# Optimization experiments

Measured on AMD Instinct MI355X. Metric: run time of the kernel, lower is better.

Reference implementation:

```python
import jax, jax.numpy as jnp
import numpy as np

B, N, C, H = 2, 8192, 256, 8  # Dh == C (attention_head_size = embedding_channels)
EPS = 1e-5  # InstanceNorm2d default eps


def setup_inputs() -> dict:
    key = jax.random.key(0)
    k1, k2, k3, k4, k5 = jax.random.split(key, 5)
    s = 1.0 / np.sqrt(C)
    return {
        "emb": jax.random.normal(k1, (B, N, C), dtype=jnp.float32),
        "Wq": jax.random.normal(k2, (C, C * H), dtype=jnp.float32) * s,
        "Wk": jax.random.normal(k3, (C, C * H), dtype=jnp.float32) * s,
        "Wv": jax.random.normal(k4, (C, C * H), dtype=jnp.float32) * s,
        "Wo": jax.random.normal(k5, (C * H, C), dtype=jnp.float32) * s,
    }


def reference(emb, Wq, Wk, Wv, Wo):
    b, n, c = emb.shape
    h = Wq.shape[1] // c  # num_heads; head_dim Dh == c

    def heads(x):  # [B,N,H*Dh] -> [B,H,N,Dh]
        return x.reshape(b, n, h, c).transpose(0, 2, 1, 3)

    qh = heads(emb @ Wq)  # [B,H,N,Dh]
    kh = heads(emb @ Wk)
    vh = heads(emb @ Wv)

    # channel attention: contract over sequence dim N -> [B,H,Dh,Dh]
    attn = jnp.einsum("bhnd,bhne->bhde", qh, kh)

    # InstanceNorm2d over the Dh x Dh map per (b,h), affine=False, biased var
    mu = attn.mean(axis=(2, 3), keepdims=True)
    var = attn.var(axis=(2, 3), keepdims=True)
    attn = (attn - mu) * jax.lax.rsqrt(var + EPS)

    attn = jax.nn.softmax(attn, axis=3)

    # attn @ v^T -> [B,H,Dh,N]
    ctx = jnp.einsum("bhde,bhne->bhdn", attn, vh)

    # permute(0,3,2,1) -> [B,N,Dh,H], flatten (Dh,H) -> KV_size
    ctx = ctx.transpose(0, 3, 2, 1).reshape(b, n, c * h)
    return ctx @ Wo  # [B,N,C]
```

## Files before the change

kernel.cpp:

```cpp
#include <hip/hip_runtime.h>
#include <hip/hip_bf16.h>

#define NB 2
#define NN 8192
#define NC 256
#define NH 8
#define NCH 2048

static constexpr float EPS = 1e-5f;


typedef __attribute__((ext_vector_type(8))) short bf16x8;
typedef __attribute__((ext_vector_type(4))) float f32x4;

#define MFMA16(a, b, c) __builtin_amdgcn_mfma_f32_16x16x32_bf16(a, b, c, 0, 0, 0)

static constexpr int ETH  = 0;
static constexpr int ETL  = 4194304;
static constexpr int WQTH = 8388608;
static constexpr int WQTL = 8912896;
static constexpr int WKTH = 9437184;
static constexpr int WKTL = 9961472;
static constexpr int WVH  = 10485760;
static constexpr int WVL  = 11010048;
static constexpr int WORH = 11534336;
static constexpr int WORL = 12058624;
static constexpr int GHH  = 12582912;
static constexpr int GHL  = 12713984;
static constexpr int T1H  = 12845056;
static constexpr int T1L  = 13893632;
static constexpr int SMH  = 14942208;
static constexpr int SML  = 15990784;
static constexpr int PTH  = 17039360;
static constexpr int PTL  = 17170432;


__device__ __forceinline__ ushort bf16rn(float x) {
    uint u = __float_as_uint(x);
    return (ushort)((u + 0x7fffu + ((u >> 16) & 1u)) >> 16);
}
__device__ __forceinline__ float bf2f(ushort h) { return __uint_as_float(((uint)h) << 16); }

__device__ __forceinline__ void stage64(ushort* __restrict__ lds, const ushort* __restrict__ src,
                                        int row0, int k0, int ld) {
    int t = threadIdx.x;
    int g = t & 7, r = t >> 3;
#pragma unroll
    for (int i = 0; i < 2; ++i, r += 32) {
        uint4 v = *(const uint4*)(src + (row0 + r) * ld + k0 + g * 8);
        *(uint4*)((char*)lds + r * 128 + ((g ^ (r & 7)) << 4)) = v;
    }
}

__device__ __forceinline__ void stage64_f32(ushort* __restrict__ ldsh, ushort* __restrict__ ldsl,
                                            const float* __restrict__ src, int row0, int k0, int ld) {
    int t = threadIdx.x;
    int g = t & 15, r = t >> 4;
#pragma unroll
    for (int i = 0; i < 4; ++i, r += 16) {
        float4 v = *(const float4*)(src + (row0 + r) * ld + k0 + g * 4);
        ushort h0 = bf16rn(v.x), h1 = bf16rn(v.y), h2 = bf16rn(v.z), h3 = bf16rn(v.w);
        ushort e0 = bf16rn(v.x - bf2f(h0)), e1 = bf16rn(v.y - bf2f(h1));
        ushort e2 = bf16rn(v.z - bf2f(h2)), e3 = bf16rn(v.w - bf2f(h3));
        int byte = r * 128 + ((((g >> 1) ^ (r & 7)) << 4) | ((g & 1) << 3));
        ushort4 hv = {h0, h1, h2, h3}, lv = {e0, e1, e2, e3};
        *(ushort4*)((char*)ldsh + byte) = hv;
        *(ushort4*)((char*)ldsl + byte) = lv;
    }
}

__device__ __forceinline__ bf16x8 frag64(const ushort* __restrict__ lds, int rbase, int ks) {
    int l = threadIdx.x & 63;
    int r = rbase + (l & 15);
    int slot = (ks * 4 + (l >> 4)) ^ (r & 7);
    return *(const bf16x8*)((const char*)lds + r * 128 + slot * 16);
}

__device__ __forceinline__ void mac3(f32x4& acc, bf16x8 ah, bf16x8 al, bf16x8 bh, bf16x8 bl) {
    acc = MFMA16(ah, bh, acc);
    acc = MFMA16(ah, bl, acc);
    acc = MFMA16(al, bh, acc);
}

__device__ __forceinline__ void mfma_tile(const ushort* Ah, const ushort* Al,
                                          const ushort* Bh, const ushort* Bl,
                                          int wm, int wn, f32x4 acc[2][2]) {
#pragma unroll
    for (int ks = 0; ks < 2; ++ks) {
        bf16x8 ah[2], al[2], bh[2], bl[2];
        ah[0] = frag64(Ah, wm, ks);      ah[1] = frag64(Ah, wm + 16, ks);
        al[0] = frag64(Al, wm, ks);      al[1] = frag64(Al, wm + 16, ks);
        bh[0] = frag64(Bh, wn, ks);      bh[1] = frag64(Bh, wn + 16, ks);
        bl[0] = frag64(Bl, wn, ks);      bl[1] = frag64(Bl, wn + 16, ks);
#pragma unroll
        for (int mi = 0; mi < 2; ++mi)
#pragma unroll
            for (int ni = 0; ni < 2; ++ni)
                mac3(acc[mi][ni], ah[mi], al[mi], bh[ni], bl[ni]);
    }
}

__device__ __forceinline__ void gemm_core(const ushort* Ahi, const ushort* Alo, int arow0, int lda, int k0a,
                                          const ushort* Bhi, const ushort* Blo, int brow0, int ldb, int k0b,
                                          int nkt, ushort* lds, f32x4 acc[2][2]) {
    ushort* Ah = lds; ushort* Al = lds + 4096; ushort* Bh = lds + 8192; ushort* Bl = lds + 12288;
    int w = threadIdx.x >> 6;
    int wm = (w >> 1) * 32, wn = (w & 1) * 32;
    for (int t = 0; t < nkt; ++t) {
        stage64(Ah, Ahi, arow0, k0a + t * 64, lda);
        stage64(Al, Alo, arow0, k0a + t * 64, lda);
        stage64(Bh, Bhi, brow0, k0b + t * 64, ldb);
        stage64(Bl, Blo, brow0, k0b + t * 64, ldb);
        __syncthreads();
        mfma_tile(Ah, Al, Bh, Bl, wm, wn, acc);
        __syncthreads();
    }
}

__device__ __forceinline__ void ep_hilo(ushort* Dh, ushort* Dl, int ld, int row0, int col0, f32x4 acc[2][2]) {
    int l = threadIdx.x & 63, w = threadIdx.x >> 6;
    int wm = (w >> 1) * 32, wn = (w & 1) * 32;
#pragma unroll
    for (int mi = 0; mi < 2; ++mi)
#pragma unroll
        for (int ni = 0; ni < 2; ++ni)
#pragma unroll
            for (int r = 0; r < 4; ++r) {
                float x = acc[mi][ni][r];
                int idx = (row0 + wm + mi * 16 + (l >> 4) * 4 + r) * ld + col0 + wn + ni * 16 + (l & 15);
                ushort h = bf16rn(x);
                Dh[idx] = h;
                Dl[idx] = bf16rn(x - bf2f(h));
            }
}

__device__ __forceinline__ void ep_f32(float* D, int ld, int row0, int col0, f32x4 acc[2][2]) {
    int l = threadIdx.x & 63, w = threadIdx.x >> 6;
    int wm = (w >> 1) * 32, wn = (w & 1) * 32;
#pragma unroll
    for (int mi = 0; mi < 2; ++mi)
#pragma unroll
        for (int ni = 0; ni < 2; ++ni)
#pragma unroll
            for (int r = 0; r < 4; ++r)
                D[(row0 + wm + mi * 16 + (l >> 4) * 4 + r) * ld + col0 + wn + ni * 16 + (l & 15)] = acc[mi][ni][r];
}

__device__ __forceinline__ void tsplit(uint (*lds)[65], const float* __restrict__ src, int srcStride,
                                       ushort* __restrict__ DH, ushort* __restrict__ DL) {
    int t = threadIdx.x;
    int r = t >> 4, g = t & 15;
#pragma unroll
    for (int i = 0; i < 4; ++i) {
        int m = r + i * 16;
        float4 v = *(const float4*)(src + m * srcStride + g * 4);
        ushort h;
        h = bf16rn(v.x); lds[g * 4 + 0][m] = h | ((uint)bf16rn(v.x - bf2f(h)) << 16);
        h = bf16rn(v.y); lds[g * 4 + 1][m] = h | ((uint)bf16rn(v.y - bf2f(h)) << 16);
        h = bf16rn(v.z); lds[g * 4 + 2][m] = h | ((uint)bf16rn(v.z - bf2f(h)) << 16);
        h = bf16rn(v.w); lds[g * 4 + 3][m] = h | ((uint)bf16rn(v.w - bf2f(h)) << 16);
    }
    __syncthreads();
    int j = t >> 3, q = t & 7;
#pragma unroll
    for (int i = 0; i < 2; ++i) {
        int jj = j + i * 32;
        uint a0 = lds[jj][q * 8 + 0], a1 = lds[jj][q * 8 + 1], a2 = lds[jj][q * 8 + 2], a3 = lds[jj][q * 8 + 3];
        uint a4 = lds[jj][q * 8 + 4], a5 = lds[jj][q * 8 + 5], a6 = lds[jj][q * 8 + 6], a7 = lds[jj][q * 8 + 7];
        uint4 hv = {(a0 & 0xffffu) | (a1 << 16), (a2 & 0xffffu) | (a3 << 16),
                    (a4 & 0xffffu) | (a5 << 16), (a6 & 0xffffu) | (a7 << 16)};
        uint4 lv = {(a0 >> 16) | (a1 & 0xffff0000u), (a2 >> 16) | (a3 & 0xffff0000u),
                    (a4 >> 16) | (a5 & 0xffff0000u), (a6 >> 16) | (a7 & 0xffff0000u)};
        *(uint4*)(DH + jj * NC + q * 8) = hv;
        *(uint4*)(DL + jj * NC + q * 8) = lv;
    }
}


__global__ __launch_bounds__(256) void k_prep(const float* __restrict__ wq, const float* __restrict__ wk,
                                              const float* __restrict__ wv, const float* __restrict__ wo,
                                              ushort* __restrict__ us, float* __restrict__ stats) {
    __shared__ uint lds[64][65];
    int x = blockIdx.x, z = blockIdx.y;
    int t = threadIdx.x;
    if (z == 3) {
        if (x == 0 && t < 64) stats[t] = 0.f;
        int i = (x * 256 + t) * 4;
        float4 v = *(const float4*)(wv + i);
        ushort h0 = bf16rn(v.x), h1 = bf16rn(v.y), h2 = bf16rn(v.z), h3 = bf16rn(v.w);
        ushort e0 = bf16rn(v.x - bf2f(h0)), e1 = bf16rn(v.y - bf2f(h1));
        ushort e2 = bf16rn(v.z - bf2f(h2)), e3 = bf16rn(v.w - bf2f(h3));
        ushort4 hv = {h0, h1, h2, h3}, lv = {e0, e1, e2, e3};
        *(ushort4*)(us + WVH + i) = hv;
        *(ushort4*)(us + WVL + i) = lv;
        return;
    }
    if (x >= 128) return;
    if (z == 2) {
        int h = x >> 4, dt = (x >> 2) & 3, jt = x & 3;
        tsplit(lds, wo + (dt * 64 * 8 + h) * NC + jt * 64, 8 * NC,
               us + WORH + h * 65536 + (jt * 64) * NC + dt * 64,
               us + WORL + h * 65536 + (jt * 64) * NC + dt * 64);
        return;
    }
    int jt = x >> 2, ct = x & 3;
    const float* W = z ? wk : wq;
    int dh = (z ? WKTH : WQTH) + (jt * 64) * NC + ct * 64;
    int dl = (z ? WKTL : WQTL) + (jt * 64) * NC + ct * 64;
    tsplit(lds, W + (ct * 64) * NCH + jt * 64, NCH, us + dh, us + dl);
}

__global__ __launch_bounds__(256) void k_s0(const float* __restrict__ emb, ushort* __restrict__ us) {
    __shared__ uint lds[64][65];
    int nt = blockIdx.x, ct = blockIdx.y, b = blockIdx.z;
    int t = threadIdx.x;
    const float* E = emb + b * (NN * NC);
    int n0 = nt * 64, c0 = ct * 64;
    int r = t >> 4, g = t & 15;
#pragma unroll
    for (int i = 0; i < 4; ++i) {
        int n = r + i * 16;
        float4 v = *(const float4*)(E + (n0 + n) * NC + c0 + g * 4);
        ushort h;
        h = bf16rn(v.x); lds[g * 4 + 0][n] = h | ((uint)bf16rn(v.x - bf2f(h)) << 16);
        h = bf16rn(v.y); lds[g * 4 + 1][n] = h | ((uint)bf16rn(v.y - bf2f(h)) << 16);
        h = bf16rn(v.z); lds[g * 4 + 2][n] = h | ((uint)bf16rn(v.z - bf2f(h)) << 16);
        h = bf16rn(v.w); lds[g * 4 + 3][n] = h | ((uint)bf16rn(v.w - bf2f(h)) << 16);
    }
    __syncthreads();
    ushort* EH = us + ETH + b * (NC * NN);
    ushort* EL = us + ETL + b * (NC * NN);
    int c = t >> 3, q = t & 7;
#pragma unroll
    for (int i = 0; i < 2; ++i) {
        int cc = c + i * 32;
        uint a0 = lds[cc][q * 8 + 0], a1 = lds[cc][q * 8 + 1], a2 = lds[cc][q * 8 + 2], a3 = lds[cc][q * 8 + 3];
        uint a4 = lds[cc][q * 8 + 4], a5 = lds[cc][q * 8 + 5], a6 = lds[cc][q * 8 + 6], a7 = lds[cc][q * 8 + 7];
        uint4 hv = {(a0 & 0xffffu) | (a1 << 16), (a2 & 0xffffu) | (a3 << 16),
                    (a4 & 0xffffu) | (a5 << 16), (a6 & 0xffffu) | (a7 << 16)};
        uint4 lv = {(a0 >> 16) | (a1 & 0xffff0000u), (a2 >> 16) | (a3 & 0xffff0000u),
                    (a4 >> 16) | (a5 & 0xffff0000u), (a6 >> 16) | (a7 & 0xffff0000u)};
        *(uint4*)(EH + (c0 + cc) * NN + n0 + q * 8) = hv;
        *(uint4*)(EL + (c0 + cc) * NN + n0 + q * 8) = lv;
    }
}

static __device__ const int TI1[10] = {0, 0, 0, 0, 1, 1, 1, 2, 2, 3};
static __device__ const int TI2[10] = {0, 1, 2, 3, 1, 2, 3, 2, 3, 3};

__global__ __launch_bounds__(256) void k_gram(const ushort* __restrict__ us, float* __restrict__ gp) {
    __shared__ ushort lds[16384];
    ushort* Ah = lds; ushort* Al = lds + 4096; ushort* Bh = lds + 8192; ushort* Bl = lds + 12288;
    int tile = blockIdx.x, kc = blockIdx.y, b = blockIdx.z;
    int c1 = TI1[tile] * 64, c2 = TI2[tile] * 64;
    bool diag = (c1 == c2);
    const ushort* eh = us + ETH + b * (NC * NN);
    const ushort* el = us + ETL + b * (NC * NN);
    int w = threadIdx.x >> 6;
    int wm = (w >> 1) * 32, wn = (w & 1) * 32;
    f32x4 acc[2][2] = {{{0.f, 0.f, 0.f, 0.f}, {0.f, 0.f, 0.f, 0.f}},
                       {{0.f, 0.f, 0.f, 0.f}, {0.f, 0.f, 0.f, 0.f}}};
    for (int kb = 0; kb < 8; ++kb) {
        int n0 = kc * 512 + kb * 64;
        stage64(Ah, eh, c1, n0, NN);
        stage64(Al, el, c1, n0, NN);
        if (!diag) { stage64(Bh, eh, c2, n0, NN); stage64(Bl, el, c2, n0, NN); }
        __syncthreads();
        mfma_tile(Ah, Al, diag ? Ah : Bh, diag ? Al : Bl, wm, wn, acc);
        __syncthreads();
    }
    ep_f32(gp + ((b * 16 + kc) * 10 + tile) * 4096, 64, 0, 0, acc);
}

__global__ __launch_bounds__(256) void k_s2(const float* __restrict__ gp, ushort* __restrict__ us) {
    __shared__ float T[64][65];
    int tile = blockIdx.x, b = blockIdx.y;
    int c1 = TI1[tile] * 64, c2 = TI2[tile] * 64;
    int t = threadIdx.x;
    const float* src = gp + (b * 160 + tile) * 4096;
    ushort* GH = us + GHH + b * 65536;
    ushort* GL = us + GHL + b * 65536;
    float4 s[4] = {{0.f, 0.f, 0.f, 0.f}, {0.f, 0.f, 0.f, 0.f}, {0.f, 0.f, 0.f, 0.f}, {0.f, 0.f, 0.f, 0.f}};
    for (int kc = 0; kc < 16; ++kc) {
        const float4* p = (const float4*)(src + kc * 40960);
#pragma unroll
        for (int k2 = 0; k2 < 4; ++k2) {
            float4 v = p[t + k2 * 256];
            s[k2].x += v.x; s[k2].y += v.y; s[k2].z += v.z; s[k2].w += v.w;
        }
    }
#pragma unroll
    for (int k2 = 0; k2 < 4; ++k2) {
        int f = t + k2 * 256;
        int r = f >> 4, c = (f & 15) * 4;
        ushort h0 = bf16rn(s[k2].x), h1 = bf16rn(s[k2].y), h2 = bf16rn(s[k2].z), h3 = bf16rn(s[k2].w);
        ushort e0 = bf16rn(s[k2].x - bf2f(h0)), e1 = bf16rn(s[k2].y - bf2f(h1));
        ushort e2 = bf16rn(s[k2].z - bf2f(h2)), e3 = bf16rn(s[k2].w - bf2f(h3));
        ushort4 hv = {h0, h1, h2, h3}, lv = {e0, e1, e2, e3};
        *(ushort4*)(GH + (c1 + r) * NC + c2 + c) = hv;
        *(ushort4*)(GL + (c1 + r) * NC + c2 + c) = lv;
        T[r][c + 0] = s[k2].x; T[r][c + 1] = s[k2].y; T[r][c + 2] = s[k2].z; T[r][c + 3] = s[k2].w;
    }
    if (c1 != c2) {
        __syncthreads();
#pragma unroll
        for (int k2 = 0; k2 < 4; ++k2) {
            int f = t + k2 * 256;
            int r = f >> 4, c = (f & 15) * 4;
            float a0 = T[c + 0][r], a1 = T[c + 1][r], a2 = T[c + 2][r], a3 = T[c + 3][r];
            ushort h0 = bf16rn(a0), h1 = bf16rn(a1), h2 = bf16rn(a2), h3 = bf16rn(a3);
            ushort e0 = bf16rn(a0 - bf2f(h0)), e1 = bf16rn(a1 - bf2f(h1));
            ushort e2 = bf16rn(a2 - bf2f(h2)), e3 = bf16rn(a3 - bf2f(h3));
            ushort4 hv = {h0, h1, h2, h3}, lv = {e0, e1, e2, e3};
            *(ushort4*)(GH + (c2 + r) * NC + c1 + c) = hv;
            *(ushort4*)(GL + (c2 + r) * NC + c1 + c) = lv;
        }
    }
}

__global__ __launch_bounds__(256) void k_t1(ushort* __restrict__ us) {
    __shared__ ushort lds[16384];
    int mt = blockIdx.x, nt = blockIdx.y, b = blockIdx.z;
    f32x4 acc[2][2] = {{{0.f, 0.f, 0.f, 0.f}, {0.f, 0.f, 0.f, 0.f}},
                       {{0.f, 0.f, 0.f, 0.f}, {0.f, 0.f, 0.f, 0.f}}};
    gemm_core(us + WQTH, us + WQTL, mt * 64, NC, 0,
              us + GHH + b * 65536, us + GHL + b * 65536, nt * 64, NC, 0, 4, lds, acc);
    ep_hilo(us + T1H + b * 524288, us + T1L + b * 524288, NC, mt * 64, nt * 64, acc);
}

__global__ __launch_bounds__(256) void k_attn(ushort* __restrict__ us, float* __restrict__ attn,
                                              float* __restrict__ stats) {
    __shared__ ushort lds[16384];
    int tile = blockIdx.x, bh = blockIdx.y;
    int b = bh >> 3, h = bh & 7;
    int row0 = (tile >> 2) * 64, col0 = (tile & 3) * 64;
    f32x4 acc[2][2] = {{{0.f, 0.f, 0.f, 0.f}, {0.f, 0.f, 0.f, 0.f}},
                       {{0.f, 0.f, 0.f, 0.f}, {0.f, 0.f, 0.f, 0.f}}};
    gemm_core(us + T1H + b * 524288, us + T1L + b * 524288, h * 256 + row0, NC, 0,
              us + WKTH, us + WKTL, h * 256 + col0, NC, 0, 4, lds, acc);
    float* D = attn + bh * 65536;
    int l = threadIdx.x & 63, w = threadIdx.x >> 6;
    int wm = (w >> 1) * 32, wn = (w & 1) * 32;
    float lsum = 0.f, lss = 0.f;
#pragma unroll
    for (int mi = 0; mi < 2; ++mi)
#pragma unroll
        for (int ni = 0; ni < 2; ++ni)
#pragma unroll
            for (int r = 0; r < 4; ++r) {
                float x = acc[mi][ni][r];
                D[(row0 + wm + mi * 16 + (l >> 4) * 4 + r) * NC + col0 + wn + ni * 16 + (l & 15)] = x;
                lsum += x; lss += x * x;
            }
#pragma unroll
    for (int o = 32; o > 0; o >>= 1) { lsum += __shfl_xor(lsum, o); lss += __shfl_xor(lss, o); }
    if (l == 0) { atomicAdd(&stats[bh * 2], lsum); atomicAdd(&stats[bh * 2 + 1], lss); }
}

__global__ __launch_bounds__(256) void k_sm(const float* __restrict__ attn, const float* __restrict__ stats,
                                            ushort* __restrict__ us) {
    int bh = blockIdx.x, rb = blockIdx.y;
    float mean = stats[bh * 2] * (1.f / 65536.f);
    float var = stats[bh * 2 + 1] * (1.f / 65536.f) - mean * mean;
    float rs = rsqrtf(var + EPS);
    int w = threadIdx.x >> 6, l = threadIdx.x & 63;
    const float* src = attn + bh * 65536;
    ushort* dh = us + SMH + bh * 65536;
    ushort* dl = us + SML + bh * 65536;
    for (int rr = 0; rr < 16; ++rr) {
        int row = rb * 64 + w * 16 + rr;
        float4 v = *(const float4*)(src + row * 256 + l * 4);
        v.x *= rs; v.y *= rs; v.z *= rs; v.w *= rs;
        float mx = fmaxf(fmaxf(v.x, v.y), fmaxf(v.z, v.w));
#pragma unroll
        for (int o = 32; o > 0; o >>= 1) mx = fmaxf(mx, __shfl_xor(mx, o));
        float e0 = __expf(v.x - mx), e1 = __expf(v.y - mx), e2 = __expf(v.z - mx), e3 = __expf(v.w - mx);
        float se = e0 + e1 + e2 + e3;
#pragma unroll
        for (int o = 32; o > 0; o >>= 1) se += __shfl_xor(se, o);
        float inv = 1.f / se;
        e0 *= inv; e1 *= inv; e2 *= inv; e3 *= inv;
        ushort h0 = bf16rn(e0), h1 = bf16rn(e1), h2 = bf16rn(e2), h3 = bf16rn(e3);
        ushort f0 = bf16rn(e0 - bf2f(h0)), f1 = bf16rn(e1 - bf2f(h1));
        ushort f2 = bf16rn(e2 - bf2f(h2)), f3 = bf16rn(e3 - bf2f(h3));
        ushort4 hv = {h0, h1, h2, h3}, lv = {f0, f1, f2, f3};
        *(ushort4*)(dh + row * 256 + l * 4) = hv;
        *(ushort4*)(dl + row * 256 + l * 4) = lv;
    }
}

__global__ __launch_bounds__(256) void k_m(ushort* __restrict__ us) {
    __shared__ ushort lds[16384];
    int tile = blockIdx.x, bh = blockIdx.y;
    int h = bh & 7;
    int c0 = (tile >> 2) * 64, d0 = (tile & 3) * 64;
    f32x4 acc[2][2] = {{{0.f, 0.f, 0.f, 0.f}, {0.f, 0.f, 0.f, 0.f}},
                       {{0.f, 0.f, 0.f, 0.f}, {0.f, 0.f, 0.f, 0.f}}};
    gemm_core(us + WVH, us + WVL, c0, NCH, h * 256,
              us + SMH + bh * 65536, us + SML + bh * 65536, d0, NC, 0, 4, lds, acc);
    ep_hilo(us + T1H + bh * 65536, us + T1L + bh * 65536, NC, c0, d0, acc);
}

__global__ __launch_bounds__(256) void k_pt(ushort* __restrict__ us, float* __restrict__ ptp) {
    __shared__ ushort lds[16384];
    int tile = blockIdx.x, bh = blockIdx.y;
    int h = bh & 7;
    int j0 = (tile >> 2) * 64, c0 = (tile & 3) * 64;
    f32x4 acc[2][2] = {{{0.f, 0.f, 0.f, 0.f}, {0.f, 0.f, 0.f, 0.f}},
                       {{0.f, 0.f, 0.f, 0.f}, {0.f, 0.f, 0.f, 0.f}}};
    gemm_core(us + WORH + h * 65536, us + WORL + h * 65536, j0, NC, 0,
              us + T1H + bh * 65536, us + T1L + bh * 65536, c0, NC, 0, 4, lds, acc);
    ep_f32(ptp + bh * 65536, NC, j0, c0, acc);
}

__global__ __launch_bounds__(256) void k_s4(const float* __restrict__ ptp, ushort* __restrict__ us) {
    int b = blockIdx.y;
    int i = (blockIdx.x * 256 + threadIdx.x) * 4;
    const float* src = ptp + b * 8 * 65536 + i;
    float4 s = {0.f, 0.f, 0.f, 0.f};
#pragma unroll
    for (int h = 0; h < 8; ++h) {
        float4 v = *(const float4*)(src + h * 65536);
        s.x += v.x; s.y += v.y; s.z += v.z; s.w += v.w;
    }
    ushort h0 = bf16rn(s.x), h1 = bf16rn(s.y), h2 = bf16rn(s.z), h3 = bf16rn(s.w);
    ushort e0 = bf16rn(s.x - bf2f(h0)), e1 = bf16rn(s.y - bf2f(h1));
    ushort e2 = bf16rn(s.z - bf2f(h2)), e3 = bf16rn(s.w - bf2f(h3));
    ushort4 hv = {h0, h1, h2, h3}, lv = {e0, e1, e2, e3};
    *(ushort4*)(us + PTH + b * 65536 + i) = hv;
    *(ushort4*)(us + PTL + b * 65536 + i) = lv;
}

__global__ __launch_bounds__(256) void k_out(const float* __restrict__ emb, const ushort* __restrict__ us,
                                             float* __restrict__ out) {
    __shared__ ushort lds[16384];
    ushort* Ah = lds; ushort* Al = lds + 4096; ushort* Bh = lds + 8192; ushort* Bl = lds + 12288;
    int nt = blockIdx.x, jt = blockIdx.y, b = blockIdx.z;
    const float* E = emb + b * (NN * NC);
    const ushort* PH = us + PTH + b * 65536;
    const ushort* PL = us + PTL + b * 65536;
    int w = threadIdx.x >> 6;
    int wm = (w >> 1) * 32, wn = (w & 1) * 32;
    f32x4 acc[2][2] = {{{0.f, 0.f, 0.f, 0.f}, {0.f, 0.f, 0.f, 0.f}},
                       {{0.f, 0.f, 0.f, 0.f}, {0.f, 0.f, 0.f, 0.f}}};
    for (int t = 0; t < 4; ++t) {
        stage64_f32(Ah, Al, E, nt * 64, t * 64, NC);
        stage64(Bh, PH, jt * 64, t * 64, NC);
        stage64(Bl, PL, jt * 64, t * 64, NC);
        __syncthreads();
        mfma_tile(Ah, Al, Bh, Bl, wm, wn, acc);
        __syncthreads();
    }
    ep_f32(out + b * (NN * NC), NC, nt * 64, jt * 64, acc);
}


extern "C" void kernel_launch(void* const* d_in, const int* in_sizes, int n_in,
                              void* d_out, int out_size, void* d_ws, size_t ws_size,
                              hipStream_t stream) {
    const float* emb = (const float*)d_in[0];
    const float* Wq  = (const float*)d_in[1];
    const float* Wk  = (const float*)d_in[2];
    const float* Wv  = (const float*)d_in[3];
    const float* Wo  = (const float*)d_in[4];
    float* out = (float*)d_out;
    float* ws  = (float*)d_ws;

    float* Gp    = ws;
    float* attn  = ws;
    float* Ptp   = ws + 1310720;
    float* stats = ws + 2359296;
    ushort* us   = (ushort*)(ws + 2359360);

    k_prep<<<dim3(512, 4),     dim3(256), 0, stream>>>(Wq, Wk, Wv, Wo, us, stats);
    k_s0  <<<dim3(128, 4, NB), dim3(256), 0, stream>>>(emb, us);
    k_gram<<<dim3(10, 16, NB), dim3(256), 0, stream>>>(us, Gp);
    k_s2  <<<dim3(10, NB),     dim3(256), 0, stream>>>(Gp, us);
    k_t1  <<<dim3(32, 4, NB),  dim3(256), 0, stream>>>(us);
    k_attn<<<dim3(16, 16),     dim3(256), 0, stream>>>(us, attn, stats);
    k_sm  <<<dim3(16, 4),      dim3(256), 0, stream>>>(attn, stats, us);
    k_m   <<<dim3(16, 16),     dim3(256), 0, stream>>>(us);
    k_pt  <<<dim3(16, 16),     dim3(256), 0, stream>>>(us, Ptp);
    k_s4  <<<dim3(64, NB),     dim3(256), 0, stream>>>(Ptp, us);
    k_out <<<dim3(128, 4, NB), dim3(256), 0, stream>>>(emb, us, out);
}
```

Before: 172.6 us.

## Use per-wave 16x16 tiles for small GEMMs, fuse emb transpose into prep, atomic head-reduce

Replaces the 64x64 LDS-staged block GEMMs for the small 256-dim stages (t1, attn, m, pt) with one 16x16 output tile per wave, reading fragments straight from global memory. This gives many more waves so the whole GPU is filled. It also folds the emb transpose/split kernel into k_prep and zeroes the new accumulator there. Per-head projections are summed with float atomics into P, which removes the Ptp buffer and the k_s4 kernel. k_out now splits P from fp32 on the fly. In exchange, fragments are loaded from global memory with no LDS reuse, the fp32 atomic sum order is nondeterministic, and k_sm's row tiling shrinks.

Result: slower. 205.7 us (+19.2%).

```diff
diff --git a/kernel.cpp b/kernel.cpp
--- a/kernel.cpp
+++ b/kernel.cpp
@@ -31,8 +31,6 @@
 static constexpr int T1L  = 13893632;
 static constexpr int SMH  = 14942208;
 static constexpr int SML  = 15990784;
-static constexpr int PTH  = 17039360;
-static constexpr int PTL  = 17170432;
 
 
 __device__ __forceinline__ ushort bf16rn(float x) {
@@ -76,10 +74,32 @@
     return *(const bf16x8*)((const char*)lds + r * 128 + slot * 16);
 }
 
+__device__ __forceinline__ bf16x8 gfrag(const ushort* __restrict__ src, int row0, int ld, int k) {
+    int l = threadIdx.x & 63;
+    return *(const bf16x8*)(src + (row0 + (l & 15)) * ld + k + (l >> 4) * 8);
+}
+
 __device__ __forceinline__ void mac3(f32x4& acc, bf16x8 ah, bf16x8 al, bf16x8 bh, bf16x8 bl) {
     acc = MFMA16(ah, bh, acc);
     acc = MFMA16(ah, bl, acc);
     acc = MFMA16(al, bh, acc);
+}
+
+template <int NK>
+__device__ __forceinline__ f32x4 wave_gemm(const ushort* __restrict__ Ah, const ushort* __restrict__ Al,
+                                           int arow0, int lda, int k0a,
+                                           const ushort* __restrict__ Bh, const ushort* __restrict__ Bl,
+                                           int brow0, int ldb, int k0b) {
+    f32x4 acc = {0.f, 0.f, 0.f, 0.f};
+#pragma unroll
+    for (int ks = 0; ks < NK; ++ks) {
+        bf16x8 ah = gfrag(Ah, arow0, lda, k0a + ks * 32);
+        bf16x8 al = gfrag(Al, arow0, lda, k0a + ks * 32);
+        bf16x8 bh = gfrag(Bh, brow0, ldb, k0b + ks * 32);
+        bf16x8 bl = gfrag(Bl, brow0, ldb, k0b + ks * 32);
+        mac3(acc, ah, al, bh, bl);
+    }
+    return acc;
 }
 
 __device__ __forceinline__ void mfma_tile(const ushort* Ah, const ushort* Al,
@@ -98,40 +118,6 @@
             for (int ni = 0; ni < 2; ++ni)
                 mac3(acc[mi][ni], ah[mi], al[mi], bh[ni], bl[ni]);
     }
-}
-
-__device__ __forceinline__ void gemm_core(const ushort* Ahi, const ushort* Alo, int arow0, int lda, int k0a,
-                                          const ushort* Bhi, const ushort* Blo, int brow0, int ldb, int k0b,
-                                          int nkt, ushort* lds, f32x4 acc[2][2]) {
-    ushort* Ah = lds; ushort* Al = lds + 4096; ushort* Bh = lds + 8192; ushort* Bl = lds + 12288;
-    int w = threadIdx.x >> 6;
-    int wm = (w >> 1) * 32, wn = (w & 1) * 32;
-    for (int t = 0; t < nkt; ++t) {
-        stage64(Ah, Ahi, arow0, k0a + t * 64, lda);
-        stage64(Al, Alo, arow0, k0a + t * 64, lda);
-        stage64(Bh, Bhi, brow0, k0b + t * 64, ldb);
-        stage64(Bl, Blo, brow0, k0b + t * 64, ldb);
-        __syncthreads();
-        mfma_tile(Ah, Al, Bh, Bl, wm, wn, acc);
-        __syncthreads();
-    }
-}
-
-__device__ __forceinline__ void ep_hilo(ushort* Dh, ushort* Dl, int ld, int row0, int col0, f32x4 acc[2][2]) {
-    int l = threadIdx.x & 63, w = threadIdx.x >> 6;
-    int wm = (w >> 1) * 32, wn = (w & 1) * 32;
-#pragma unroll
-    for (int mi = 0; mi < 2; ++mi)
-#pragma unroll
-        for (int ni = 0; ni < 2; ++ni)
-#pragma unroll
-            for (int r = 0; r < 4; ++r) {
-                float x = acc[mi][ni][r];
-                int idx = (row0 + wm + mi * 16 + (l >> 4) * 4 + r) * ld + col0 + wn + ni * 16 + (l & 15);
-                ushort h = bf16rn(x);
-                Dh[idx] = h;
-                Dl[idx] = bf16rn(x - bf2f(h));
-            }
 }
 
 __device__ __forceinline__ void ep_f32(float* D, int ld, int row0, int col0, f32x4 acc[2][2]) {
@@ -179,12 +165,47 @@
 
 __global__ __launch_bounds__(256) void k_prep(const float* __restrict__ wq, const float* __restrict__ wk,
                                               const float* __restrict__ wv, const float* __restrict__ wo,
-                                              ushort* __restrict__ us, float* __restrict__ stats) {
+                                              const float* __restrict__ emb, ushort* __restrict__ us,
+                                              float* __restrict__ P, float* __restrict__ stats) {
     __shared__ uint lds[64][65];
     int x = blockIdx.x, z = blockIdx.y;
     int t = threadIdx.x;
+    if (z >= 4) {
+        int b = z - 4, nt = x >> 2, ct = x & 3;
+        const float* E = emb + b * (NN * NC);
+        int n0 = nt * 64, c0 = ct * 64;
+        int r = t >> 4, g = t & 15;
+#pragma unroll
+        for (int i = 0; i < 4; ++i) {
+            int n = r + i * 16;
+            float4 v = *(const float4*)(E + (n0 + n) * NC + c0 + g * 4);
+            ushort h;
+            h = bf16rn(v.x); lds[g * 4 + 0][n] = h | ((uint)bf16rn(v.x - bf2f(h)) << 16);
+            h = bf16rn(v.y); lds[g * 4 + 1][n] = h | ((uint)bf16rn(v.y - bf2f(h)) << 16);
+            h = bf16rn(v.z); lds[g * 4 + 2][n] = h | ((uint)bf16rn(v.z - bf2f(h)) << 16);
+            h = bf16rn(v.w); lds[g * 4 + 3][n] = h | ((uint)bf16rn(v.w - bf2f(h)) << 16);
+        }
+        __syncthreads();
+        ushort* EH = us + ETH + b * (NC * NN);
+        ushort* EL = us + ETL + b * (NC * NN);
+        int c = t >> 3, q = t & 7;
+#pragma unroll
+        for (int i = 0; i < 2; ++i) {
+            int cc = c + i * 32;
+            uint a0 = lds[cc][q * 8 + 0], a1 = lds[cc][q * 8 + 1], a2 = lds[cc][q * 8 + 2], a3 = lds[cc][q * 8 + 3];
+            uint a4 = lds[cc][q * 8 + 4], a5 = lds[cc][q * 8 + 5], a6 = lds[cc][q * 8 + 6], a7 = lds[cc][q * 8 + 7];
+            uint4 hv = {(a0 & 0xffffu) | (a1 << 16), (a2 & 0xffffu) | (a3 << 16),
+                        (a4 & 0xffffu) | (a5 << 16), (a6 & 0xffffu) | (a7 << 16)};
+            uint4 lv = {(a0 >> 16) | (a1 & 0xffff0000u), (a2 >> 16) | (a3 & 0xffff0000u),
+                        (a4 >> 16) | (a5 & 0xffff0000u), (a6 >> 16) | (a7 & 0xffff0000u)};
+            *(uint4*)(EH + (c0 + cc) * NN + n0 + q * 8) = hv;
+            *(uint4*)(EL + (c0 + cc) * NN + n0 + q * 8) = lv;
+        }
+        return;
+    }
     if (z == 3) {
         if (x == 0 && t < 64) stats[t] = 0.f;
+        P[x * 256 + t] = 0.f;
         int i = (x * 256 + t) * 4;
         float4 v = *(const float4*)(wv + i);
         ushort h0 = bf16rn(v.x), h1 = bf16rn(v.y), h2 = bf16rn(v.z), h3 = bf16rn(v.w);
@@ -208,41 +229,6 @@
     int dh = (z ? WKTH : WQTH) + (jt * 64) * NC + ct * 64;
     int dl = (z ? WKTL : WQTL) + (jt * 64) * NC + ct * 64;
     tsplit(lds, W + (ct * 64) * NCH + jt * 64, NCH, us + dh, us + dl);
-}
-
-__global__ __launch_bounds__(256) void k_s0(const float* __restrict__ emb, ushort* __restrict__ us) {
-    __shared__ uint lds[64][65];
-    int nt = blockIdx.x, ct = blockIdx.y, b = blockIdx.z;
-    int t = threadIdx.x;
-    const float* E = emb + b * (NN * NC);
-    int n0 = nt * 64, c0 = ct * 64;
-    int r = t >> 4, g = t & 15;
-#pragma unroll
-    for (int i = 0; i < 4; ++i) {
-        int n = r + i * 16;
-        float4 v = *(const float4*)(E + (n0 + n) * NC + c0 + g * 4);
-        ushort h;
-        h = bf16rn(v.x); lds[g * 4 + 0][n] = h | ((uint)bf16rn(v.x - bf2f(h)) << 16);
-        h = bf16rn(v.y); lds[g * 4 + 1][n] = h | ((uint)bf16rn(v.y - bf2f(h)) << 16);
-        h = bf16rn(v.z); lds[g * 4 + 2][n] = h | ((uint)bf16rn(v.z - bf2f(h)) << 16);
-        h = bf16rn(v.w); lds[g * 4 + 3][n] = h | ((uint)bf16rn(v.w - bf2f(h)) << 16);
-    }
-    __syncthreads();
-    ushort* EH = us + ETH + b * (NC * NN);
-    ushort* EL = us + ETL + b * (NC * NN);
-    int c = t >> 3, q = t & 7;
-#pragma unroll
-    for (int i = 0; i < 2; ++i) {
-        int cc = c + i * 32;
-        uint a0 = lds[cc][q * 8 + 0], a1 = lds[cc][q * 8 + 1], a2 = lds[cc][q * 8 + 2], a3 = lds[cc][q * 8 + 3];
-        uint a4 = lds[cc][q * 8 + 4], a5 = lds[cc][q * 8 + 5], a6 = lds[cc][q * 8 + 6], a7 = lds[cc][q * 8 + 7];
-        uint4 hv = {(a0 & 0xffffu) | (a1 << 16), (a2 & 0xffffu) | (a3 << 16),
-                    (a4 & 0xffffu) | (a5 << 16), (a6 & 0xffffu) | (a7 << 16)};
-        uint4 lv = {(a0 >> 16) | (a1 & 0xffff0000u), (a2 >> 16) | (a3 & 0xffff0000u),
-                    (a4 >> 16) | (a5 & 0xffff0000u), (a6 >> 16) | (a7 & 0xffff0000u)};
-        *(uint4*)(EH + (c0 + cc) * NN + n0 + q * 8) = hv;
-        *(uint4*)(EL + (c0 + cc) * NN + n0 + q * 8) = lv;
-    }
 }
 
 static __device__ const int TI1[10] = {0, 0, 0, 0, 1, 1, 1, 2, 2, 3};
@@ -318,43 +304,51 @@
     }
 }
 
-__global__ __launch_bounds__(256) void k_t1(ushort* __restrict__ us) {
-    __shared__ ushort lds[16384];
-    int mt = blockIdx.x, nt = blockIdx.y, b = blockIdx.z;
-    f32x4 acc[2][2] = {{{0.f, 0.f, 0.f, 0.f}, {0.f, 0.f, 0.f, 0.f}},
-                       {{0.f, 0.f, 0.f, 0.f}, {0.f, 0.f, 0.f, 0.f}}};
-    gemm_core(us + WQTH, us + WQTL, mt * 64, NC, 0,
-              us + GHH + b * 65536, us + GHL + b * 65536, nt * 64, NC, 0, 4, lds, acc);
-    ep_hilo(us + T1H + b * 524288, us + T1L + b * 524288, NC, mt * 64, nt * 64, acc);
-}
-
-__global__ __launch_bounds__(256) void k_attn(ushort* __restrict__ us, float* __restrict__ attn,
-                                              float* __restrict__ stats) {
-    __shared__ ushort lds[16384];
-    int tile = blockIdx.x, bh = blockIdx.y;
+__global__ __launch_bounds__(256) void k_t1w(ushort* __restrict__ us) {
+    int wid = blockIdx.x * 4 + (threadIdx.x >> 6);
+    int b = wid >> 11, rem = wid & 2047;
+    int rt = rem >> 4, ct = rem & 15;
+    f32x4 acc = wave_gemm<8>(us + WQTH, us + WQTL, rt * 16, NC, 0,
+                             us + GHH + b * 65536, us + GHL + b * 65536, ct * 16, NC, 0);
+    int l = threadIdx.x & 63;
+    ushort* Dh = us + T1H + b * 524288;
+    ushort* Dl = us + T1L + b * 524288;
+#pragma unroll
+    for (int r = 0; r < 4; ++r) {
+        float x = acc[r];
+        int idx = (rt * 16 + (l >> 4) * 4 + r) * NC + ct * 16 + (l & 15);
+        ushort h = bf16rn(x);
+        Dh[idx] = h;
+        Dl[idx] = bf16rn(x - bf2f(h));
+    }
+}
+
+__global__ __launch_bounds__(256) void k_attnw(const ushort* __restrict__ us, float* __restrict__ attn,
+                                               float* __restrict__ stats) {
+    __shared__ float red[8];
+    int w = threadIdx.x >> 6, l = threadIdx.x & 63;
+    int bh = blockIdx.x >> 6;
+    int tile = (blockIdx.x & 63) * 4 + w;
+    int dt = tile >> 4, et = tile & 15;
     int b = bh >> 3, h = bh & 7;
-    int row0 = (tile >> 2) * 64, col0 = (tile & 3) * 64;
-    f32x4 acc[2][2] = {{{0.f, 0.f, 0.f, 0.f}, {0.f, 0.f, 0.f, 0.f}},
-                       {{0.f, 0.f, 0.f, 0.f}, {0.f, 0.f, 0.f, 0.f}}};
-    gemm_core(us + T1H + b * 524288, us + T1L + b * 524288, h * 256 + row0, NC, 0,
-              us + WKTH, us + WKTL, h * 256 + col0, NC, 0, 4, lds, acc);
+    f32x4 acc = wave_gemm<8>(us + T1H + b * 524288, us + T1L + b * 524288, h * 256 + dt * 16, NC, 0,
+                             us + WKTH, us + WKTL, h * 256 + et * 16, NC, 0);
     float* D = attn + bh * 65536;
-    int l = threadIdx.x & 63, w = threadIdx.x >> 6;
-    int wm = (w >> 1) * 32, wn = (w & 1) * 32;
-    float lsum = 0.f, lss = 0.f;
-#pragma unroll
-    for (int mi = 0; mi < 2; ++mi)
-#pragma unroll
-        for (int ni = 0; ni < 2; ++ni)
-#pragma unroll
-            for (int r = 0; r < 4; ++r) {
-                float x = acc[mi][ni][r];
-                D[(row0 + wm + mi * 16 + (l >> 4) * 4 + r) * NC + col0 + wn + ni * 16 + (l & 15)] = x;
-                lsum += x; lss += x * x;
-            }
-#pragma unroll
-    for (int o = 32; o > 0; o >>= 1) { lsum += __shfl_xor(lsum, o); lss += __shfl_xor(lss, o); }
-    if (l == 0) { atomicAdd(&stats[bh * 2], lsum); atomicAdd(&stats[bh * 2 + 1], lss); }
+    float s = 0.f, ss = 0.f;
+#pragma unroll
+    for (int r = 0; r < 4; ++r) {
+        float x = acc[r];
+        D[(dt * 16 + (l >> 4) * 4 + r) * NC + et * 16 + (l & 15)] = x;
+        s += x; ss += x * x;
+    }
+#pragma unroll
+    for (int o = 32; o > 0; o >>= 1) { s += __shfl_xor(s, o); ss += __shfl_xor(ss, o); }
+    if (l == 0) { red[w] = s; red[4 + w] = ss; }
+    __syncthreads();
+    if (threadIdx.x == 0) {
+        atomicAdd(&stats[bh * 2], red[0] + red[1] + red[2] + red[3]);
+        atomicAdd(&stats[bh * 2 + 1], red[4] + red[5] + red[6] + red[7]);
+    }
 }
 
 __global__ __launch_bounds__(256) void k_sm(const float* __restrict__ attn, const float* __restrict__ stats,
@@ -367,8 +361,9 @@
     const float* src = attn + bh * 65536;
     ushort* dh = us + SMH + bh * 65536;
     ushort* dl = us + SML + bh * 65536;
-    for (int rr = 0; rr < 16; ++rr) {
-        int row = rb * 64 + w * 16 + rr;
+#pragma unroll
+    for (int rr = 0; rr < 4; ++rr) {
+        int row = rb * 16 + w * 4 + rr;
         float4 v = *(const float4*)(src + row * 256 + l * 4);
         v.x *= rs; v.y *= rs; v.z *= rs; v.w *= rs;
         float mx = fmaxf(fmaxf(v.x, v.y), fmaxf(v.z, v.w));
@@ -389,64 +384,54 @@
     }
 }
 
-__global__ __launch_bounds__(256) void k_m(ushort* __restrict__ us) {
-    __shared__ ushort lds[16384];
-    int tile = blockIdx.x, bh = blockIdx.y;
+__global__ __launch_bounds__(256) void k_mw(ushort* __restrict__ us) {
+    int wid = blockIdx.x * 4 + (threadIdx.x >> 6);
+    int bh = wid >> 8, rem = wid & 255;
+    int ct = rem >> 4, dt = rem & 15;
     int h = bh & 7;
-    int c0 = (tile >> 2) * 64, d0 = (tile & 3) * 64;
-    f32x4 acc[2][2] = {{{0.f, 0.f, 0.f, 0.f}, {0.f, 0.f, 0.f, 0.f}},
-                       {{0.f, 0.f, 0.f, 0.f}, {0.f, 0.f, 0.f, 0.f}}};
-    gemm_core(us + WVH, us + WVL, c0, NCH, h * 256,
-              us + SMH + bh * 65536, us + SML + bh * 65536, d0, NC, 0, 4, lds, acc);
-    ep_hilo(us + T1H + bh * 65536, us + T1L + bh * 65536, NC, c0, d0, acc);
-}
-
-__global__ __launch_bounds__(256) void k_pt(ushort* __restrict__ us, float* __restrict__ ptp) {
-    __shared__ ushort lds[16384];
-    int tile = blockIdx.x, bh = blockIdx.y;
-    int h = bh & 7;
-    int j0 = (tile >> 2) * 64, c0 = (tile & 3) * 64;
-    f32x4 acc[2][2] = {{{0.f, 0.f, 0.f, 0.f}, {0.f, 0.f, 0.f, 0.f}},
-                       {{0.f, 0.f, 0.f, 0.f}, {0.f, 0.f, 0.f, 0.f}}};
-    gemm_core(us + WORH + h * 65536, us + WORL + h * 65536, j0, NC, 0,
-              us + T1H + bh * 65536, us + T1L + bh * 65536, c0, NC, 0, 4, lds, acc);
-    ep_f32(ptp + bh * 65536, NC, j0, c0, acc);
-}
-
-__global__ __launch_bounds__(256) void k_s4(const float* __restrict__ ptp, ushort* __restrict__ us) {
-    int b = blockIdx.y;
-    int i = (blockIdx.x * 256 + threadIdx.x) * 4;
-    const float* src = ptp + b * 8 * 65536 + i;
-    float4 s = {0.f, 0.f, 0.f, 0.f};
-#pragma unroll
-    for (int h = 0; h < 8; ++h) {
-        float4 v = *(const float4*)(src + h * 65536);
-        s.x += v.x; s.y += v.y; s.z += v.z; s.w += v.w;
-    }
-    ushort h0 = bf16rn(s.x), h1 = bf16rn(s.y), h2 = bf16rn(s.z), h3 = bf16rn(s.w);
-    ushort e0 = bf16rn(s.x - bf2f(h0)), e1 = bf16rn(s.y - bf2f(h1));
-    ushort e2 = bf16rn(s.z - bf2f(h2)), e3 = bf16rn(s.w - bf2f(h3));
-    ushort4 hv = {h0, h1, h2, h3}, lv = {e0, e1, e2, e3};
-    *(ushort4*)(us + PTH + b * 65536 + i) = hv;
-    *(ushort4*)(us + PTL + b * 65536 + i) = lv;
-}
-
-__global__ __launch_bounds__(256) void k_out(const float* __restrict__ emb, const ushort* __restrict__ us,
+    f32x4 acc = wave_gemm<8>(us + WVH, us + WVL, ct * 16, NCH, h * 256,
+                             us + SMH + bh * 65536, us + SML + bh * 65536, dt * 16, NC, 0);
+    int l = threadIdx.x & 63;
+    ushort* Dh = us + T1H + bh * 65536;
+    ushort* Dl = us + T1L + bh * 65536;
+#pragma unroll
+    for (int r = 0; r < 4; ++r) {
+        float x = acc[r];
+        int idx = (ct * 16 + (l >> 4) * 4 + r) * NC + dt * 16 + (l & 15);
+        ushort hh = bf16rn(x);
+        Dh[idx] = hh;
+        Dl[idx] = bf16rn(x - bf2f(hh));
+    }
+}
+
+__global__ __launch_bounds__(256) void k_ptw(const ushort* __restrict__ us, float* __restrict__ P) {
+    int wid = blockIdx.x * 4 + (threadIdx.x >> 6);
+    int bh = wid >> 8, rem = wid & 255;
+    int jt = rem >> 4, ct = rem & 15;
+    int b = bh >> 3, h = bh & 7;
+    f32x4 acc = wave_gemm<8>(us + WORH + h * 65536, us + WORL + h * 65536, jt * 16, NC, 0,
+                             us + T1H + bh * 65536, us + T1L + bh * 65536, ct * 16, NC, 0);
+    int l = threadIdx.x & 63;
+    float* D = P + b * 65536;
+#pragma unroll
+    for (int r = 0; r < 4; ++r)
+        atomicAdd(&D[(jt * 16 + (l >> 4) * 4 + r) * NC + ct * 16 + (l & 15)], acc[r]);
+}
+
+__global__ __launch_bounds__(256) void k_out(const float* __restrict__ emb, const float* __restrict__ P,
                                              float* __restrict__ out) {
     __shared__ ushort lds[16384];
     ushort* Ah = lds; ushort* Al = lds + 4096; ushort* Bh = lds + 8192; ushort* Bl = lds + 12288;
     int nt = blockIdx.x, jt = blockIdx.y, b = blockIdx.z;
     const float* E = emb + b * (NN * NC);
-    const ushort* PH = us + PTH + b * 65536;
-    const ushort* PL = us + PTL + b * 65536;
+    const float* Pb = P + b * 65536;
     int w = threadIdx.x >> 6;
     int wm = (w >> 1) * 32, wn = (w & 1) * 32;
     f32x4 acc[2][2] = {{{0.f, 0.f, 0.f, 0.f}, {0.f, 0.f, 0.f, 0.f}},
                        {{0.f, 0.f, 0.f, 0.f}, {0.f, 0.f, 0.f, 0.f}}};
     for (int t = 0; t < 4; ++t) {
         stage64_f32(Ah, Al, E, nt * 64, t * 64, NC);
-        stage64(Bh, PH, jt * 64, t * 64, NC);
-        stage64(Bl, PL, jt * 64, t * 64, NC);
+        stage64_f32(Bh, Bl, Pb, jt * 64, t * 64, NC);
         __syncthreads();
         mfma_tile(Ah, Al, Bh, Bl, wm, wn, acc);
         __syncthreads();
@@ -468,19 +453,17 @@
 
     float* Gp    = ws;
     float* attn  = ws;
-    float* Ptp   = ws + 1310720;
-    float* stats = ws + 2359296;
-    ushort* us   = (ushort*)(ws + 2359360);
-
-    k_prep<<<dim3(512, 4),     dim3(256), 0, stream>>>(Wq, Wk, Wv, Wo, us, stats);
-    k_s0  <<<dim3(128, 4, NB), dim3(256), 0, stream>>>(emb, us);
-    k_gram<<<dim3(10, 16, NB), dim3(256), 0, stream>>>(us, Gp);
-    k_s2  <<<dim3(10, NB),     dim3(256), 0, stream>>>(Gp, us);
-    k_t1  <<<dim3(32, 4, NB),  dim3(256), 0, stream>>>(us);
-    k_attn<<<dim3(16, 16),     dim3(256), 0, stream>>>(us, attn, stats);
-    k_sm  <<<dim3(16, 4),      dim3(256), 0, stream>>>(attn, stats, us);
-    k_m   <<<dim3(16, 16),     dim3(256), 0, stream>>>(us);
-    k_pt  <<<dim3(16, 16),     dim3(256), 0, stream>>>(us, Ptp);
-    k_s4  <<<dim3(64, NB),     dim3(256), 0, stream>>>(Ptp, us);
-    k_out <<<dim3(128, 4, NB), dim3(256), 0, stream>>>(emb, us, out);
-}
+    float* P     = ws + 1310720;
+    float* stats = ws + 1441792;
+    ushort* us   = (ushort*)(ws + 1441856);
+
+    k_prep <<<dim3(512, 6),     dim3(256), 0, stream>>>(Wq, Wk, Wv, Wo, emb, us, P, stats);
+    k_gram <<<dim3(10, 16, NB), dim3(256), 0, stream>>>(us, Gp);
+    k_s2   <<<dim3(10, NB),     dim3(256), 0, stream>>>(Gp, us);
+    k_t1w  <<<dim3(1024),       dim3(256), 0, stream>>>(us);
+    k_attnw<<<dim3(1024),       dim3(256), 0, stream>>>(us, attn, stats);
+    k_sm   <<<dim3(16, 16),     dim3(256), 0, stream>>>(attn, stats, us);
+    k_mw   <<<dim3(1024),       dim3(256), 0, stream>>>(us);
+    k_ptw  <<<dim3(1024),       dim3(256), 0, stream>>>(us, P);
+    k_out  <<<dim3(128, 4, NB), dim3(256), 0, stream>>>(emb, P, out);
+}
```
